# Performance work log

Hardware: AMD Instinct MI355X
Metric: run time of the kernel (lower is better)

## Reference

```python
import math
import jax, jax.numpy as jnp
import numpy as np

INPUT_SIZE = 168; PREDICT_SIZE = 168; D_MODEL = 512; D_FF = 512
WINDOW = [4, 4, 4]; INNER = 3; N_HEADS = 6; D_K = 128; N_LAYER = 6
ENC_IN = 7; D_BOTTLE = 128; T_FEAT = 4
H = N_HEADS * D_K  # 768


def _all_sizes():
    s = [INPUT_SIZE]
    for w in WINDOW:
        s.append(s[-1] // w)
    return s  # [168, 42, 10, 2]


def _enc_mask():
    # Pyraformer PAM mask: True = masked (disallowed)
    all_size = _all_sizes()
    S = sum(all_size)
    m = np.zeros((S, S), dtype=bool)
    iw = INNER // 2
    starts = np.concatenate([[0], np.cumsum(all_size)]).astype(int)
    # intra-scale neighbors
    for li, n in enumerate(all_size):
        st = starts[li]
        for i in range(st, st + n):
            l = max(i - iw, st)
            r = min(i + iw + 1, st + n)
            m[i, l:r] = True
    # inter-scale parent/child links (symmetric)
    for li in range(1, len(all_size)):
        st = starts[li]
        prev = all_size[li - 1]
        for i in range(st, st + all_size[li]):
            l = (st - prev) + (i - st) * WINDOW[li - 1]
            if i == st + all_size[li] - 1:
                r = st
            else:
                r = (st - prev) + (i - st + 1) * WINDOW[li - 1]
            m[i, l:r] = True
            m[l:r, i] = True
    return jnp.asarray(~m)


def _dec_mask():
    # get_subsequent_mask(truncate=False): query i sees all 222 encoder tokens + dec tokens 0..i
    S = sum(_all_sizes())
    q = np.arange(PREDICT_SIZE)[:, None]
    k = np.arange(S + PREDICT_SIZE)[None, :]
    return jnp.asarray(k > S + q)  # True = masked


def _pos_emb(L):
    pos = np.arange(L, dtype=np.float32)[:, None]
    div = np.exp(np.arange(0, D_MODEL, 2, dtype=np.float32) * (-math.log(10000.0) / D_MODEL))
    pe = np.zeros((L, D_MODEL), np.float32)
    pe[:, 0::2] = np.sin(pos * div)
    pe[:, 1::2] = np.cos(pos * div)
    return jnp.asarray(pe)


def _ln(x, g, b, eps):
    m = jnp.mean(x, -1, keepdims=True)
    v = jnp.mean((x - m) ** 2, -1, keepdims=True)
    return (x - m) * jax.lax.rsqrt(v + eps) * g + b


def _embed(x, t, conv_w, tw, tb):
    # TokenEmbedding: Conv1d(k=3, circular pad, no bias) + positional + TimeFeature linear
    xt = jnp.transpose(x, (0, 2, 1))  # [B,C,L]
    xt = jnp.pad(xt, ((0, 0), (0, 0), (1, 1)), mode='wrap')
    tok = jax.lax.conv_general_dilated(xt, conv_w, (1,), 'VALID',
                                       dimension_numbers=('NCH', 'OIH', 'NCH'))
    tok = jnp.transpose(tok, (0, 2, 1))  # [B,L,D]
    return tok + _pos_emb(x.shape[1])[None] + t @ tw + tb


def _mha(q_in, kv, wq, bq, wk, bk, wv, bv, wo, bo, g, b, mask):
    B, Lq, _ = q_in.shape
    Lk = kv.shape[1]
    q = (q_in @ wq + bq).reshape(B, Lq, N_HEADS, D_K)
    k = (kv @ wk + bk).reshape(B, Lk, N_HEADS, D_K)
    v = (kv @ wv + bv).reshape(B, Lk, N_HEADS, D_K)
    attn = jnp.einsum('bqhd,bkhd->bhqk', q, k) / math.sqrt(D_K)
    attn = jnp.where(mask[None, None], -1e9, attn)
    attn = jax.nn.softmax(attn, axis=-1)
    out = jnp.einsum('bhqk,bkhd->bqhd', attn, v).reshape(B, Lq, H)
    return _ln(out @ wo + bo + q_in, g, b, 1e-6)


def _ffn(x, w1, b1, w2, b2, g, b):
    h = jax.nn.gelu(x @ w1 + b1, approximate=False)
    return _ln(h @ w2 + b2 + x, g, b, 1e-6)


def _bottleneck(x, dw, db, cw, cb, bng, bnb, bnm, bnv, uw, ub, lg, lb):
    # Bottleneck_Construct: down-proj, stack of strided convs (one per window), up-proj, concat, LN
    tmp = jnp.transpose(x @ dw + db, (0, 2, 1))  # [B,128,L]
    outs = []
    for i in range(len(WINDOW)):
        tmp = jax.lax.conv_general_dilated(tmp, cw[i], (WINDOW[i],), 'VALID',
                                           dimension_numbers=('NCH', 'OIH', 'NCH'))
        tmp = tmp + cb[i][None, :, None]
        # BatchNorm1d in eval mode (running stats)
        tmp = (tmp - bnm[i][None, :, None]) * jax.lax.rsqrt(bnv[i][None, :, None] + 1e-5)
        tmp = tmp * bng[i][None, :, None] + bnb[i][None, :, None]
        tmp = jax.nn.elu(tmp)
        outs.append(tmp)
    cat = jnp.transpose(jnp.concatenate(outs, axis=2), (0, 2, 1))  # [B,54,128]
    up = cat @ uw + ub
    return _ln(jnp.concatenate([x, up], axis=1), lg, lb, 1e-5)  # [B,222,512]


def _forward(p):
    mask_e = _enc_mask()
    enc = _embed(p['x_enc'], p['t_enc'], p['enc_tok_w'], p['enc_time_w'], p['enc_time_b'])
    enc = _bottleneck(enc, p['bc_down_w'], p['bc_down_b'], p['bc_conv_w'], p['bc_conv_b'],
                      p['bc_bn_g'], p['bc_bn_b'], p['bc_bn_m'], p['bc_bn_v'],
                      p['bc_up_w'], p['bc_up_b'], p['bc_ln_g'], p['bc_ln_b'])
    for i in range(N_LAYER):
        enc = _mha(enc, enc, p['enc_wq'][i], p['enc_bq'][i], p['enc_wk'][i], p['enc_bk'][i],
                   p['enc_wv'][i], p['enc_bv'][i], p['enc_wo'][i], p['enc_bo'][i],
                   p['enc_ln1_g'][i], p['enc_ln1_b'][i], mask_e)
        enc = _ffn(enc, p['enc_w1'][i], p['enc_b1'][i], p['enc_w2'][i], p['enc_b2'][i],
                   p['enc_ln2_g'][i], p['enc_ln2_b'][i])
    dec = _embed(p['x_dec'], p['t_dec'], p['dec_tok_w'], p['dec_time_w'], p['dec_time_b'])
    mask_d = _dec_mask()
    for i in range(2):
        kv = jnp.concatenate([enc, dec], axis=1)  # [B,390,D]
        dec = _mha(dec, kv, p['dec_wq'][i], p['dec_bq'][i], p['dec_wk'][i], p['dec_bk'][i],
                   p['dec_wv'][i], p['dec_bv'][i], p['dec_wo'][i], p['dec_bo'][i],
                   p['dec_ln1_g'][i], p['dec_ln1_b'][i], mask_d)
        dec = _ffn(dec, p['dec_w1'][i], p['dec_b1'][i], p['dec_w2'][i], p['dec_b2'][i],
                   p['dec_ln2_g'][i], p['dec_ln2_b'][i])
    if p['pretrain']:
        dec = jnp.concatenate([p_enc_trunc(dec, p), dec], axis=1)
    return dec @ p['pred_w']


def setup_inputs() -> dict:
    key = jax.random.key(0)
    cnt = [0]
    def nrm(shape, s=0.02):
        cnt[0] += 1
        return jax.random.normal(jax.random.fold_in(key, cnt[0]), shape, jnp.float32) * s
    B = 64
    d = {
        'x_enc': nrm((B, INPUT_SIZE, ENC_IN), 1.0),
        't_enc': nrm((B, INPUT_SIZE, T_FEAT), 1.0),
        'x_dec': nrm((B, PREDICT_SIZE, ENC_IN), 1.0),
        't_dec': nrm((B, PREDICT_SIZE, T_FEAT), 1.0),
        'enc_tok_w': nrm((D_MODEL, ENC_IN, 3)),
        'enc_time_w': nrm((T_FEAT, D_MODEL)), 'enc_time_b': jnp.zeros((D_MODEL,), jnp.float32),
        'dec_tok_w': nrm((D_MODEL, ENC_IN, 3)),
        'dec_time_w': nrm((T_FEAT, D_MODEL)), 'dec_time_b': jnp.zeros((D_MODEL,), jnp.float32),
        'bc_down_w': nrm((D_MODEL, D_BOTTLE)), 'bc_down_b': jnp.zeros((D_BOTTLE,), jnp.float32),
        'bc_conv_w': nrm((3, D_BOTTLE, D_BOTTLE, 4)), 'bc_conv_b': jnp.zeros((3, D_BOTTLE), jnp.float32),
        'bc_bn_g': jnp.ones((3, D_BOTTLE), jnp.float32), 'bc_bn_b': jnp.zeros((3, D_BOTTLE), jnp.float32),
        'bc_bn_m': jnp.zeros((3, D_BOTTLE), jnp.float32), 'bc_bn_v': jnp.ones((3, D_BOTTLE), jnp.float32),
        'bc_up_w': nrm((D_BOTTLE, D_MODEL)), 'bc_up_b': jnp.zeros((D_MODEL,), jnp.float32),
        'bc_ln_g': jnp.ones((D_MODEL,), jnp.float32), 'bc_ln_b': jnp.zeros((D_MODEL,), jnp.float32),
    }
    for prefix, n in (('enc_', N_LAYER), ('dec_', 2)):
        d[prefix + 'wq'] = nrm((n, D_MODEL, H)); d[prefix + 'bq'] = jnp.zeros((n, H), jnp.float32)
        d[prefix + 'wk'] = nrm((n, D_MODEL, H)); d[prefix + 'bk'] = jnp.zeros((n, H), jnp.float32)
        d[prefix + 'wv'] = nrm((n, D_MODEL, H)); d[prefix + 'bv'] = jnp.zeros((n, H), jnp.float32)
        d[prefix + 'wo'] = nrm((n, H, D_MODEL)); d[prefix + 'bo'] = jnp.zeros((n, D_MODEL), jnp.float32)
        d[prefix + 'ln1_g'] = jnp.ones((n, D_MODEL), jnp.float32); d[prefix + 'ln1_b'] = jnp.zeros((n, D_MODEL), jnp.float32)
        d[prefix + 'w1'] = nrm((n, D_MODEL, D_FF)); d[prefix + 'b1'] = jnp.zeros((n, D_FF), jnp.float32)
        d[prefix + 'w2'] = nrm((n, D_FF, D_MODEL)); d[prefix + 'b2'] = jnp.zeros((n, D_MODEL), jnp.float32)
        d[prefix + 'ln2_g'] = jnp.ones((n, D_MODEL), jnp.float32); d[prefix + 'ln2_b'] = jnp.zeros((n, D_MODEL), jnp.float32)
    d['pred_w'] = nrm((D_MODEL, ENC_IN))
    d['pretrain'] = 0
    return d


def reference(x_enc, t_enc, x_dec, t_dec, enc_tok_w, enc_time_w, enc_time_b, dec_tok_w, dec_time_w, dec_time_b, bc_down_w, bc_down_b, bc_conv_w, bc_conv_b, bc_bn_g, bc_bn_b, bc_bn_m, bc_bn_v, bc_up_w, bc_up_b, bc_ln_g, bc_ln_b, enc_wq, enc_bq, enc_wk, enc_bk, enc_wv, enc_bv, enc_wo, enc_bo, enc_ln1_g, enc_ln1_b, enc_w1, enc_b1, enc_w2, enc_b2, enc_ln2_g, enc_ln2_b, dec_wq, dec_bq, dec_wk, dec_bk, dec_wv, dec_bv, dec_wo, dec_bo, dec_ln1_g, dec_ln1_b, dec_w1, dec_b1, dec_w2, dec_b2, dec_ln2_g, dec_ln2_b, pred_w, pretrain):
    p = dict(locals())
    return _forward(p)
```

## Files before the change

kernel.cpp:

```cpp
#include <hip/hip_runtime.h>
#include <cstdint>
#include <cstddef>

#define BSZ   64
#define L_IN  168
#define S1    222
#define SKV   390
#define DM    512
#define HD    768
#define NHD   6
#define DK    128

typedef unsigned short u16;
typedef unsigned int u32;
typedef __attribute__((ext_vector_type(8))) short bf16x8;
typedef __attribute__((ext_vector_type(4))) float f32x4v;

__device__ inline float b2f(u16 u){
  union { u32 i; float f; } v; v.i = ((u32)u) << 16; return v.f;
}
__device__ inline u16 f2b(float f){
  union { float f; u32 i; } v; v.f = f;
  u32 x = v.i;
  return (u16)((x + 0x7fffu + ((x >> 16) & 1u)) >> 16);
}
__device__ inline u32 pk2(float a, float b){
  return ((u32)f2b(b) << 16) | (u32)f2b(a);
}
__device__ inline float ldv(const void* p, long long i, bool f32){
  return f32 ? ((const float*)p)[i] : b2f(((const u16*)p)[i]);
}
__device__ inline float4 ldv4(const void* p, long long i, bool f32){
  if (f32) return *(const float4*)((const float*)p + i);
  ushort4 w = *(const ushort4*)((const u16*)p + i);
  return make_float4(b2f(w.x), b2f(w.y), b2f(w.z), b2f(w.w));
}
__device__ inline bool is_f32(const u16* det){ return det[0] != 0x3F80; }
__device__ inline void unpack8(uint4 w, float* f){
  union { u32 i; float fl; } a;
  a.i = w.x << 16;          f[0] = a.fl;
  a.i = w.x & 0xffff0000u;  f[1] = a.fl;
  a.i = w.y << 16;          f[2] = a.fl;
  a.i = w.y & 0xffff0000u;  f[3] = a.fl;
  a.i = w.z << 16;          f[4] = a.fl;
  a.i = w.z & 0xffff0000u;  f[5] = a.fl;
  a.i = w.w << 16;          f[6] = a.fl;
  a.i = w.w & 0xffff0000u;  f[7] = a.fl;
}

__device__ inline void gload_lds16(const void* g, void* l){
  __builtin_amdgcn_global_load_lds((const __attribute__((address_space(1))) void*)g,
                                   (__attribute__((address_space(3))) void*)l, 16, 0, 0);
}

constexpr size_t OFF_ENCX = 0;
constexpr size_t OFF_DECX = OFF_ENCX + (size_t)BSZ*S1*DM;
constexpr size_t OFF_QB   = OFF_DECX + (size_t)BSZ*L_IN*DM;
constexpr size_t OFF_KB   = OFF_QB   + (size_t)BSZ*S1*HD/2;
constexpr size_t OFF_VB   = OFF_KB   + (size_t)BSZ*SKV*HD/2;
constexpr size_t OFF_NBR  = OFF_VB   + (size_t)BSZ*SKV*HD/2;
constexpr size_t OFF_ENCB = OFF_NBR  + 4096;
constexpr size_t OFF_DECB = OFF_ENCB + (size_t)BSZ*S1*DM/2;
constexpr size_t OFF_WT   = OFF_DECB + (size_t)BSZ*L_IN*DM/2;
constexpr size_t WT_SLOT  = 2097152;
constexpr size_t WS_NEED  = (OFF_WT) * 4;
constexpr size_t WS_NEED2 = (OFF_WT + 8*WT_SLOT/2) * 4;

__device__ inline int scale_of(int i, int& ii){
  if (i < 168){ ii = i;       return 0; }
  if (i < 210){ ii = i - 168; return 1; }
  if (i < 220){ ii = i - 210; return 2; }
  ii = i - 220; return 3;
}
__device__ inline bool pam_ok(int i, int j){
  int ii, jj;
  int li = scale_of(i, ii);
  int lj = scale_of(j, jj);
  const int n[4] = {168, 42, 10, 2};
  if (li == lj){ int d = ii - jj; return (d <= 1 && d >= -1); }
  if (li == lj + 1){ int lo = ii*4, hi = (ii == n[li]-1) ? n[lj] : ii*4+4; return (jj >= lo && jj < hi); }
  if (lj == li + 1){ int lo = jj*4, hi = (jj == n[lj]-1) ? n[li] : jj*4+4; return (ii >= lo && ii < hi); }
  return false;
}
__global__ __launch_bounds__(256)
void build_nbr_kernel(int* __restrict__ nbr){
  int wid = (blockIdx.x * 256 + threadIdx.x) >> 6;
  int lane = threadIdx.x & 63;
  if (wid >= S1) return;
  int q = wid;
  int cnt = 0;
  int list[12];
  #pragma unroll
  for (int r = 0; r < 4; ++r){
    int j = r*64 + lane;
    bool ok = (j < S1) && pam_ok(q, j);
    unsigned long long m = __ballot(ok);
    while (m && cnt < 12){
      int bit = __builtin_ctzll(m);
      m &= m - 1;
      list[cnt++] = r*64 + bit;
    }
  }
  if (lane == 0){
    #pragma unroll
    for (int t = 0; t < 12; ++t) nbr[q*12 + t] = (t < cnt) ? list[t] : -1;
  }
}

__global__ __launch_bounds__(256)
void embed_fast(const void* __restrict__ x, const void* __restrict__ t,
                const void* __restrict__ cw, const void* __restrict__ tw,
                const void* __restrict__ tb, const u16* __restrict__ det,
                float* __restrict__ out, u16* __restrict__ out2)
{
  bool f32 = is_f32(det);
  int d0 = threadIdx.x;
  int d1 = threadIdx.x + 256;

  float w0[21], w1[21];
  #pragma unroll
  for (int i = 0; i < 21; ++i){
    w0[i] = ldv(cw, (long long)d0*21 + i, f32);
    w1[i] = ldv(cw, (long long)d1*21 + i, f32);
  }
  float tw0[4], tw1[4];
  #pragma unroll
  for (int f = 0; f < 4; ++f){
    tw0[f] = ldv(tw, (long long)f*DM + d0, f32);
    tw1[f] = ldv(tw, (long long)f*DM + d1, f32);
  }
  float tb0 = ldv(tb, d0, f32);
  float tb1 = ldv(tb, d1, f32);
  float dv0 = __expf(-(float)(d0 & ~1) * (9.210340371976184f/512.f));
  float dv1 = __expf(-(float)(d1 & ~1) * (9.210340371976184f/512.f));
  bool odd0 = (d0 & 1), odd1 = (d1 & 1);

  const int nRows = BSZ * L_IN;
  for (int row = blockIdx.x; row < nRows; row += gridDim.x){
    int b = row / L_IN, l = row - b*L_IN;
    float acc0 = 0.f, acc1 = 0.f;
    #pragma unroll
    for (int tt = 0; tt < 3; ++tt){
      int ls = l + tt - 1;
      ls = (ls < 0) ? ls + L_IN : (ls >= L_IN ? ls - L_IN : ls);
      long long xo = ((long long)(b*L_IN + ls))*7;
      #pragma unroll
      for (int c = 0; c < 7; ++c){
        float xv = ldv(x, xo + c, f32);
        acc0 += xv * w0[c*3 + tt];
        acc1 += xv * w1[c*3 + tt];
      }
    }
    float ang0 = (float)l * dv0;
    float ang1 = (float)l * dv1;
    acc0 += odd0 ? __cosf(ang0) : __sinf(ang0);
    acc1 += odd1 ? __cosf(ang1) : __sinf(ang1);
    long long to = ((long long)row)*4;
    #pragma unroll
    for (int f = 0; f < 4; ++f){
      float tv = ldv(t, to + f, f32);
      acc0 += tv * tw0[f];
      acc1 += tv * tw1[f];
    }
    acc0 += tb0;
    acc1 += tb1;
    size_t o = (size_t)row*DM;
    out[o + d0] = acc0;
    out[o + d1] = acc1;
    if (out2){
      out2[o + d0] = f2b(acc0);
      out2[o + d1] = f2b(acc1);
    }
  }
}

__device__ inline void trans32(const void* W, long long wOff, int K, int N, int k0, int n0,
                               u16* __restrict__ Wt, bool f32, float* tb, int tid)
{
  int c = tid & 31, r0 = tid >> 5;
  #pragma unroll
  for (int rr = 0; rr < 32; rr += 8)
    tb[(r0+rr)*33 + c] = ldv(W, wOff + (long long)(k0+r0+rr)*N + n0 + c, f32);
  __syncthreads();
  #pragma unroll
  for (int rr = 0; rr < 32; rr += 8)
    Wt[(size_t)(n0+r0+rr)*K + k0 + c] = f2b(tb[c*33 + r0+rr]);
}

__device__ inline void wt_layer_body(int t, const void* wq, const void* wk, const void* wv,
                                     const void* wo, const void* w1, const void* w2,
                                     long long wO, long long oO, long long fO,
                                     u16* Wt3, u16* WtO, u16* Wt1, u16* Wt2,
                                     bool f32, float* tb, int tid)
{
  if (t < 384)       trans32(wq, wO, 512, 768, (t/24)*32, (t%24)*32, Wt3,               f32, tb, tid);
  else if (t < 768)  { int u = t-384;  trans32(wk, wO, 512, 768, (u/24)*32, (u%24)*32, Wt3 + (size_t)768*512,  f32, tb, tid); }
  else if (t < 1152) { int u = t-768;  trans32(wv, wO, 512, 768, (u/24)*32, (u%24)*32, Wt3 + (size_t)1536*512, f32, tb, tid); }
  else if (t < 1536) { int u = t-1152; trans32(wo, oO, 768, 512, (u/16)*32, (u%16)*32, WtO, f32, tb, tid); }
  else if (t < 1792) { int u = t-1536; trans32(w1, fO, 512, 512, (u/16)*32, (u%16)*32, Wt1, f32, tb, tid); }
  else               { int u = t-1792; trans32(w2, fO, 512, 512, (u/16)*32, (u%16)*32, Wt2, f32, tb, tid); }
}

__global__ __launch_bounds__(256)
void wt_batch(const void* wq, const void* wk, const void* wv,
              const void* wo, const void* w1, const void* w2,
              long long wO, long long oO, long long fO,
              u16* __restrict__ Wt3, u16* __restrict__ WtO,
              u16* __restrict__ Wt1, u16* __restrict__ Wt2,
              const u16* __restrict__ det)
{
  __shared__ float tb[32*33];
  bool f32 = is_f32(det);
  wt_layer_body(blockIdx.x, wq, wk, wv, wo, w1, w2, wO, oO, fO, Wt3, WtO, Wt1, Wt2,
                f32, tb, threadIdx.x);
}

__global__ __launch_bounds__(256)
void wt_all(const void* ewq, const void* ewk, const void* ewv, const void* ewo,
            const void* ew1, const void* ew2,
            const void* dwq, const void* dwk, const void* dwv, const void* dwo,
            const void* dw1, const void* dw2,
            u16* __restrict__ WtAll, const u16* __restrict__ det)
{
  __shared__ float tb[32*33];
  bool f32 = is_f32(det);
  int s = blockIdx.x >> 11;
  int t = blockIdx.x & 2047;
  bool enc = s < 6;
  int li = enc ? s : s - 6;
  long long wO = (long long)li*512*768, oO = (long long)li*768*512, fO = (long long)li*512*512;
  u16* base = WtAll + (size_t)s*WT_SLOT;
  wt_layer_body(t,
                enc ? ewq : dwq, enc ? ewk : dwk, enc ? ewv : dwv,
                enc ? ewo : dwo, enc ? ew1 : dw1, enc ? ew2 : dw2,
                wO, oO, fO,
                base, base + (size_t)2304*512,
                base + (size_t)2304*512 + (size_t)512*768,
                base + (size_t)2304*512 + (size_t)512*768 + (size_t)512*512,
                f32, tb, threadIdx.x);
}

template<int CN>
__device__ inline bool swzT(int t, int RP, int CP, int rpx, int& row0, int& col0){
  int xcd = t & 7, j = t >> 3;
  int rp = xcd + 8*(j % rpx);
  int cp = j / rpx;
  if (rp >= RP || cp >= CP) return false;
  row0 = rp*128; col0 = cp*CN;
  return true;
}

template<int EPI, int ABF, int CBF, int CN>
__global__ __launch_bounds__(256)
void gemm_mfma(const void* __restrict__ Av, const u16* __restrict__ Wt,
               const void* __restrict__ bias, long long bOff, const float* __restrict__ R,
               void* __restrict__ Cv, const u16* __restrict__ det,
               int K, int N, int La, int Lc, int off, int RP, int CP, int rpx)
{
  constexpr int NF = CN/32;
  __shared__ u16 As[128][64];
  __shared__ u16 Bs[CN][64];
  bool f32 = is_f32(det);
  int tid = threadIdx.x;
  int row0, col0;
  if (!swzT<CN>(blockIdx.x, RP, CP, rpx, row0, col0)) return;
  int wave = tid >> 6, lane = tid & 63;
  int wm = (wave >> 1)*64, wn = (wave & 1)*(CN/2);
  int lm = lane & 15, quad = lane >> 4;
  int sr = tid >> 1;
  int sh = (tid & 1) * 32;
  int swzS = (sr & 7) * 8;
  int r8 = lane >> 3;
  int scw = ((lane & 7)*8) ^ (r8*8);
  f32x4v acc[4][NF];
  #pragma unroll
  for (int i = 0; i < 4; ++i)
    #pragma unroll
    for (int j = 0; j < NF; ++j) acc[i][j] = (f32x4v){0.f,0.f,0.f,0.f};

  for (int k0 = 0; k0 < K; k0 += 64){
    if (ABF){
      const u16* base = (const u16*)Av + (size_t)row0*K + k0 + scw;
      #pragma unroll
      for (int j = 0; j < 4; ++j){
        int r = wave*32 + j*8;
        gload_lds16(base + (size_t)(r + r8)*K, &As[r][0]);
      }
    } else {
      const float* src = (const float*)Av + (size_t)(row0+sr)*K + k0 + sh;
      #pragma unroll
      for (int j = 0; j < 4; ++j){
        float4 f0 = *(const float4*)(src + 8*j);
        float4 f1 = *(const float4*)(src + 8*j + 4);
        uint4 o;
        o.x = pk2(f0.x, f0.y); o.y = pk2(f0.z, f0.w);
        o.z = pk2(f1.x, f1.y); o.w = pk2(f1.z, f1.w);
        *(uint4*)&As[sr][(sh + 8*j)^swzS] = o;
      }
    }
    {
      const u16* base = Wt + (size_t)col0*K + k0 + scw;
      #pragma unroll
      for (int j = 0; j < CN/32; ++j){
        int r = wave*(CN/4) + j*8;
        gload_lds16(base + (size_t)(r + r8)*K, &Bs[r][0]);
      }
    }
    __syncthreads();
    bf16x8 af[4][2], bfr[NF][2];
    #pragma unroll
    for (int mi = 0; mi < 4; ++mi){
      int m = wm + mi*16 + lm;
      int sz = (m & 7)*8;
      af[mi][0] = *(const bf16x8*)&As[m][(quad*8) ^ sz];
      af[mi][1] = *(const bf16x8*)&As[m][(32 + quad*8) ^ sz];
    }
    #pragma unroll
    for (int ni = 0; ni < NF; ++ni){
      int n = wn + ni*16 + lm;
      int sz = (n & 7)*8;
      bfr[ni][0] = *(const bf16x8*)&Bs[n][(quad*8) ^ sz];
      bfr[ni][1] = *(const bf16x8*)&Bs[n][(32 + quad*8) ^ sz];
    }
    #pragma unroll
    for (int mi = 0; mi < 4; ++mi)
      #pragma unroll
      for (int ni = 0; ni < NF; ++ni){
        acc[mi][ni] = __builtin_amdgcn_mfma_f32_16x16x32_bf16(af[mi][0], bfr[ni][0], acc[mi][ni], 0, 0, 0);
        acc[mi][ni] = __builtin_amdgcn_mfma_f32_16x16x32_bf16(af[mi][1], bfr[ni][1], acc[mi][ni], 0, 0, 0);
      }
    __syncthreads();
  }
  #pragma unroll
  for (int mi = 0; mi < 4; ++mi){
    #pragma unroll
    for (int r = 0; r < 4; ++r){
      int row = row0 + wm + mi*16 + quad*4 + r;
      int bb = row / La, l = row - bb*La;
      size_t crow = ((size_t)bb*Lc + off + l)*(size_t)N;
      #pragma unroll
      for (int ni = 0; ni < NF; ++ni){
        int col = col0 + wn + ni*16 + lm;
        float vv = acc[mi][ni][r] + ldv(bias, bOff + col, f32);
        if (EPI == 1) vv = 0.5f*vv*(1.f + erff(vv*0.70710678118654752f));
        if (EPI == 2) vv += R[crow + col];
        if (CBF) ((u16*)Cv)[crow + col] = f2b(vv);
        else     ((float*)Cv)[crow + col] = vv;
      }
    }
  }
}

template<int ABF, int CN>
__global__ __launch_bounds__(256)
void gemm_qkv(const void* __restrict__ Av, const u16* __restrict__ Wt,
              const void* __restrict__ b0, const void* __restrict__ b1, const void* __restrict__ b2,
              long long bOff, u16* __restrict__ o0, u16* __restrict__ o1, u16* __restrict__ o2,
              const u16* __restrict__ det, int La, int Lc, int off, int RP, int CP, int rpx)
{
  constexpr int NF = CN/32;
  __shared__ u16 As[128][64];
  __shared__ u16 Bs[CN][64];
  bool f32 = is_f32(det);
  const int K = 512;
  int tid = threadIdx.x;
  int row0, col0;
  if (!swzT<CN>(blockIdx.x, RP, CP, rpx, row0, col0)) return;
  int wave = tid >> 6, lane = tid & 63;
  int wm = (wave >> 1)*64, wn = (wave & 1)*(CN/2);
  int lm = lane & 15, quad = lane >> 4;
  int sr = tid >> 1;
  int sh = (tid & 1) * 32;
  int swzS = (sr & 7) * 8;
  int r8 = lane >> 3;
  int scw = ((lane & 7)*8) ^ (r8*8);
  f32x4v acc[4][NF];
  #pragma unroll
  for (int i = 0; i < 4; ++i)
    #pragma unroll
    for (int j = 0; j < NF; ++j) acc[i][j] = (f32x4v){0.f,0.f,0.f,0.f};

  for (int k0 = 0; k0 < K; k0 += 64){
    if (ABF){
      const u16* base = (const u16*)Av + (size_t)row0*K + k0 + scw;
      #pragma unroll
      for (int j = 0; j < 4; ++j){
        int r = wave*32 + j*8;
        gload_lds16(base + (size_t)(r + r8)*K, &As[r][0]);
      }
    } else {
      const float* src = (const float*)Av + (size_t)(row0+sr)*K + k0 + sh;
      #pragma unroll
      for (int j = 0; j < 4; ++j){
        float4 f0 = *(const float4*)(src + 8*j);
        float4 f1 = *(const float4*)(src + 8*j + 4);
        uint4 o;
        o.x = pk2(f0.x, f0.y); o.y = pk2(f0.z, f0.w);
        o.z = pk2(f1.x, f1.y); o.w = pk2(f1.z, f1.w);
        *(uint4*)&As[sr][(sh + 8*j)^swzS] = o;
      }
    }
    {
      const u16* base = Wt + (size_t)col0*K + k0 + scw;
      #pragma unroll
      for (int j = 0; j < CN/32; ++j){
        int r = wave*(CN/4) + j*8;
        gload_lds16(base + (size_t)(r + r8)*K, &Bs[r][0]);
      }
    }
    __syncthreads();
    bf16x8 af[4][2], bfr[NF][2];
    #pragma unroll
    for (int mi = 0; mi < 4; ++mi){
      int m = wm + mi*16 + lm;
      int sz = (m & 7)*8;
      af[mi][0] = *(const bf16x8*)&As[m][(quad*8) ^ sz];
      af[mi][1] = *(const bf16x8*)&As[m][(32 + quad*8) ^ sz];
    }
    #pragma unroll
    for (int ni = 0; ni < NF; ++ni){
      int n = wn + ni*16 + lm;
      int sz = (n & 7)*8;
      bfr[ni][0] = *(const bf16x8*)&Bs[n][(quad*8) ^ sz];
      bfr[ni][1] = *(const bf16x8*)&Bs[n][(32 + quad*8) ^ sz];
    }
    #pragma unroll
    for (int mi = 0; mi < 4; ++mi)
      #pragma unroll
      for (int ni = 0; ni < NF; ++ni){
        acc[mi][ni] = __builtin_amdgcn_mfma_f32_16x16x32_bf16(af[mi][0], bfr[ni][0], acc[mi][ni], 0, 0, 0);
        acc[mi][ni] = __builtin_amdgcn_mfma_f32_16x16x32_bf16(af[mi][1], bfr[ni][1], acc[mi][ni], 0, 0, 0);
      }
    __syncthreads();
  }
  #pragma unroll
  for (int mi = 0; mi < 4; ++mi){
    #pragma unroll
    for (int r = 0; r < 4; ++r){
      int row = row0 + wm + mi*16 + quad*4 + r;
      int bb = row / La, l = row - bb*La;
      size_t crow = ((size_t)bb*Lc + off + l)*(size_t)HD;
      #pragma unroll
      for (int ni = 0; ni < NF; ++ni){
        int col = col0 + wn + ni*16 + lm;
        int sel = (col >= 1536) ? 2 : (col >= 768 ? 1 : 0);
        int colr = col - sel*768;
        const void* bp = (sel == 0) ? b0 : (sel == 1) ? b1 : b2;
        u16* dst = (sel == 0) ? o0 : (sel == 1) ? o1 : o2;
        float vv = acc[mi][ni][r] + ldv(bp, bOff + colr, f32);
        dst[crow + colr] = f2b(vv);
      }
    }
  }
}

#define BM 64
#define BN 64
#define BK 16
__global__ __launch_bounds__(256)
void gemm_k(const float* __restrict__ A, const void* __restrict__ W, long long wOff,
            const void* __restrict__ bias, long long bOff,
            float* __restrict__ C, const u16* __restrict__ det, int K, int N)
{
  __shared__ float As2[BK][BM+4];
  __shared__ float Bs2[BK][BN+4];
  bool f32 = is_f32(det);
  int tid = threadIdx.x;
  int row0 = blockIdx.y * BM, col0 = blockIdx.x * BN;
  int ty = tid >> 4, tx = tid & 15;
  int lr = tid >> 2, lc4 = (tid & 3) << 2;
  int wr = tid >> 4, wc4 = (tid & 15) << 2;
  float acc[4][4] = {};
  for (int k0 = 0; k0 < K; k0 += BK){
    float4 av = *(const float4*)(A + (size_t)(row0 + lr)*K + k0 + lc4);
    As2[lc4+0][lr] = av.x; As2[lc4+1][lr] = av.y;
    As2[lc4+2][lr] = av.z; As2[lc4+3][lr] = av.w;
    float4 wv = ldv4(W, wOff + (long long)(k0 + wr)*N + col0 + wc4, f32);
    *(float4*)&Bs2[wr][wc4] = wv;
    __syncthreads();
    #pragma unroll
    for (int kk = 0; kk < BK; ++kk){
      float4 a  = *(const float4*)&As2[kk][ty << 2];
      float4 bb = *(const float4*)&Bs2[kk][tx << 2];
      acc[0][0] += a.x*bb.x; acc[0][1] += a.x*bb.y; acc[0][2] += a.x*bb.z; acc[0][3] += a.x*bb.w;
      acc[1][0] += a.y*bb.x; acc[1][1] += a.y*bb.y; acc[1][2] += a.y*bb.z; acc[1][3] += a.y*bb.w;
      acc[2][0] += a.z*bb.x; acc[2][1] += a.z*bb.y; acc[2][2] += a.z*bb.z; acc[2][3] += a.z*bb.w;
      acc[3][0] += a.w*bb.x; acc[3][1] += a.w*bb.y; acc[3][2] += a.w*bb.z; acc[3][3] += a.w*bb.w;
    }
    __syncthreads();
  }
  #pragma unroll
  for (int i = 0; i < 4; ++i){
    int r = row0 + (ty << 2) + i;
    size_t crow = (size_t)r*(size_t)N;
    #pragma unroll
    for (int j = 0; j < 4; ++j){
      int c = col0 + (tx << 2) + j;
      C[crow + c] = acc[i][j] + ldv(bias, bOff + c, f32);
    }
  }
}

__global__ void wc_kernel(const void* __restrict__ w, float* __restrict__ Wc,
                          const u16* __restrict__ det)
{
  bool f32 = is_f32(det);
  int idx = blockIdx.x * 256 + threadIdx.x;
  if (idx >= 3*512*128) return;
  int co = idx & 127;
  int kk = (idx >> 7) & 511;
  int lay = idx >> 16;
  int tt = kk >> 7, ci = kk & 127;
  Wc[idx] = ldv(w, (long long)lay*65536 + co*512 + ci*4 + tt, f32);
}

__global__ __launch_bounds__(256)
void conv_gemm(const float* __restrict__ in, int inStride, int inOff,
               float* __restrict__ out, int outStride, int outOff, int Lout,
               const float* __restrict__ Wc,
               const void* __restrict__ cb, const void* __restrict__ bg,
               const void* __restrict__ bb, const void* __restrict__ bm,
               const void* __restrict__ bv, const u16* __restrict__ det, int lay)
{
  __shared__ float As2[BK][BM+4];
  __shared__ float Bs2[BK][BN+4];
  bool f32 = is_f32(det);
  int tid = threadIdx.x;
  int row0 = blockIdx.y * BM, col0 = blockIdx.x * BN;
  int ty = tid >> 4, tx = tid & 15;
  int lr = tid >> 2, lc4 = (tid & 3) << 2;
  int wr = tid >> 4, wc4 = (tid & 15) << 2;
  int rs = row0 + lr;
  int bs = rs / Lout, js = rs - bs*Lout;
  const float* arow = in + ((size_t)(bs*inStride + inOff + js*4))*128;
  float acc[4][4] = {};
  for (int k0 = 0; k0 < 512; k0 += BK){
    float4 av = *(const float4*)(arow + k0 + lc4);
    As2[lc4+0][lr] = av.x; As2[lc4+1][lr] = av.y;
    As2[lc4+2][lr] = av.z; As2[lc4+3][lr] = av.w;
    float4 wv = *(const float4*)(Wc + (size_t)(k0 + wr)*128 + col0 + wc4);
    *(float4*)&Bs2[wr][wc4] = wv;
    __syncthreads();
    #pragma unroll
    for (int kk = 0; kk < BK; ++kk){
      float4 a  = *(const float4*)&As2[kk][ty << 2];
      float4 bb2 = *(const float4*)&Bs2[kk][tx << 2];
      acc[0][0] += a.x*bb2.x; acc[0][1] += a.x*bb2.y; acc[0][2] += a.x*bb2.z; acc[0][3] += a.x*bb2.w;
      acc[1][0] += a.y*bb2.x; acc[1][1] += a.y*bb2.y; acc[1][2] += a.y*bb2.z; acc[1][3] += a.y*bb2.w;
      acc[2][0] += a.z*bb2.x; acc[2][1] += a.z*bb2.y; acc[2][2] += a.z*bb2.z; acc[2][3] += a.z*bb2.w;
      acc[3][0] += a.w*bb2.x; acc[3][1] += a.w*bb2.y; acc[3][2] += a.w*bb2.z; acc[3][3] += a.w*bb2.w;
    }
    __syncthreads();
  }
  #pragma unroll
  for (int i = 0; i < 4; ++i){
    int r = row0 + (ty << 2) + i;
    int b = r / Lout, j = r - b*Lout;
    float* orow = out + ((size_t)(b*outStride + outOff + j))*128;
    #pragma unroll
    for (int jj = 0; jj < 4; ++jj){
      int co = col0 + (tx << 2) + jj;
      long long po = (long long)lay*128 + co;
      float a = acc[i][jj] + ldv(cb, po, f32);
      a = (a - ldv(bm, po, f32)) * rsqrtf(ldv(bv, po, f32) + 1e-5f) * ldv(bg, po, f32) + ldv(bb, po, f32);
      a = a > 0.f ? a : (__expf(a) - 1.f);
      orow[co] = a;
    }
  }
}

__global__ __launch_bounds__(256)
void ln_kernel(const float* __restrict__ X, const void* __restrict__ g, long long gOff,
               const void* __restrict__ bt, long long bOff, float eps,
               float* __restrict__ Out, u16* __restrict__ OutB, const u16* __restrict__ det)
{
  bool f32 = is_f32(det);
  int row = blockIdx.x*4 + (threadIdx.x >> 6);
  int lane = threadIdx.x & 63;
  const float* xr = X + (size_t)row*DM;
  float v[8]; float s = 0.f;
  #pragma unroll
  for (int i = 0; i < 8; ++i){ v[i] = xr[lane + i*64]; s += v[i]; }
  #pragma unroll
  for (int o = 32; o > 0; o >>= 1) s += __shfl_xor(s, o);
  float mean = s * (1.f/512.f);
  float q = 0.f;
  #pragma unroll
  for (int i = 0; i < 8; ++i){ float d = v[i]-mean; q += d*d; }
  #pragma unroll
  for (int o = 32; o > 0; o >>= 1) q += __shfl_xor(q, o);
  float inv = rsqrtf(q*(1.f/512.f) + eps);
  float* orow = Out + (size_t)row*DM;
  #pragma unroll
  for (int i = 0; i < 8; ++i){
    int c = lane + i*64;
    float val = (v[i]-mean)*inv*ldv(g, gOff + c, f32) + ldv(bt, bOff + c, f32);
    orow[c] = val;
    if (OutB) OutB[(size_t)row*DM + c] = f2b(val);
  }
}

__global__ __launch_bounds__(256)
void concat_ln_kernel(const float* __restrict__ emb, const float* __restrict__ up,
                      const void* __restrict__ g, const void* __restrict__ bt,
                      float* __restrict__ Out, u16* __restrict__ OutB, const u16* __restrict__ det)
{
  bool f32 = is_f32(det);
  int row = blockIdx.x*4 + (threadIdx.x >> 6);
  int lane = threadIdx.x & 63;
  int b = row / S1, l = row - b*S1;
  const float* xr = (l < L_IN) ? emb + ((size_t)(b*L_IN + l))*DM
                               : up  + ((size_t)(b*54 + (l - L_IN)))*DM;
  float v[8]; float s = 0.f;
  #pragma unroll
  for (int i = 0; i < 8; ++i){ v[i] = xr[lane + i*64]; s += v[i]; }
  #pragma unroll
  for (int o = 32; o > 0; o >>= 1) s += __shfl_xor(s, o);
  float mean = s * (1.f/512.f);
  float q = 0.f;
  #pragma unroll
  for (int i = 0; i < 8; ++i){ float d = v[i]-mean; q += d*d; }
  #pragma unroll
  for (int o = 32; o > 0; o >>= 1) q += __shfl_xor(q, o);
  float inv = rsqrtf(q*(1.f/512.f) + 1e-5f);
  float* orow = Out + (size_t)row*DM;
  #pragma unroll
  for (int i = 0; i < 8; ++i){
    int c = lane + i*64;
    float val = (v[i]-mean)*inv*ldv(g, c, f32) + ldv(bt, c, f32);
    orow[c] = val;
    if (OutB) OutB[(size_t)row*DM + c] = f2b(val);
  }
}

__global__ __launch_bounds__(256)
void attn_enc_sparse(u16* __restrict__ q, const u16* __restrict__ k,
                     const u16* __restrict__ v, const int* __restrict__ nbr)
{
  int u = blockIdx.x * 16 + (threadIdx.x >> 4);
  int lane16 = threadIdx.x & 15;
  int h = u % NHD;
  int bq = u / NHD;
  int b = bq / S1, qr = bq - b*S1;
  const float scale = 0.088388347648318447f;
  size_t rowoff = (size_t)bq*HD + h*DK + lane16*8;
  uint4 qw = *(const uint4*)(q + rowoff);
  float qd[8]; unpack8(qw, qd);
  const int* nb = nbr + qr*12;
  size_t base = (size_t)b*S1*HD + h*DK + lane16*8;
  float pj[12];
  #pragma unroll
  for (int j = 0; j < 12; ++j){
    int kg = nb[j];
    int kgc = kg < 0 ? 0 : kg;
    uint4 kw = *(const uint4*)(k + (size_t)kgc*HD + base);
    float kd[8]; unpack8(kw, kd);
    float p = qd[0]*kd[0] + qd[1]*kd[1] + qd[2]*kd[2] + qd[3]*kd[3]
            + qd[4]*kd[4] + qd[5]*kd[5] + qd[6]*kd[6] + qd[7]*kd[7];
    p += __shfl_xor(p, 1); p += __shfl_xor(p, 2);
    p += __shfl_xor(p, 4); p += __shfl_xor(p, 8);
    pj[j] = (kg >= 0) ? p*scale : -1e30f;
  }
  float m = -1e30f;
  #pragma unroll
  for (int j = 0; j < 12; ++j) m = fmaxf(m, pj[j]);
  float s = 0.f;
  #pragma unroll
  for (int j = 0; j < 12; ++j){ pj[j] = __expf(pj[j] - m); s += pj[j]; }
  float inv = 1.f / s;
  float o[8];
  #pragma unroll
  for (int i = 0; i < 8; ++i) o[i] = 0.f;
  #pragma unroll
  for (int j = 0; j < 12; ++j){
    int kg = nb[j];
    int kgc = kg < 0 ? 0 : kg;
    uint4 vw = *(const uint4*)(v + (size_t)kgc*HD + base);
    float vd[8]; unpack8(vw, vd);
    #pragma unroll
    for (int i = 0; i < 8; ++i) o[i] += pj[j]*vd[i];
  }
  uint4 ow;
  ow.x = pk2(o[0]*inv, o[1]*inv);
  ow.y = pk2(o[2]*inv, o[3]*inv);
  ow.z = pk2(o[4]*inv, o[5]*inv);
  ow.w = pk2(o[6]*inv, o[7]*inv);
  *(uint4*)(q + rowoff) = ow;
}

#define FQT 64
__global__ __launch_bounds__(256)
void attn_dec_mfma(u16* __restrict__ q, const u16* __restrict__ k,
                   const u16* __restrict__ v)
{
  __shared__ __align__(16) u16 Ks[32][136];
  __shared__ __align__(16) u32 Vt[16][132];
  __shared__ __align__(16) u32 Pls[4][16][16];
  int id = blockIdx.x;
  int qt = id / 384;
  int rem = id - qt*384;
  int h = rem >> 6;
  int b = rem & 63;
  int qt0 = qt * FQT;
  int tid = threadIdx.x;
  int wave = tid >> 6, lane = tid & 63;
  int lm = lane & 15, quad = lane >> 4;
  const float scale = 0.088388347648318447f;
  const size_t qb0 = (size_t)b*L_IN*HD + (size_t)h*DK;
  const size_t kb0 = (size_t)b*SKV*HD + (size_t)h*DK;

  bf16x8 qf[4];
  {
    int qg = qt0 + wave*16 + lm;
    if (qg < L_IN){
      #pragma unroll
      for (int ks = 0; ks < 4; ++ks)
        qf[ks] = *(const bf16x8*)(q + qb0 + (size_t)qg*HD + ks*32 + quad*8);
    } else {
      #pragma unroll
      for (int ks = 0; ks < 4; ++ks) qf[ks] = (bf16x8){0,0,0,0,0,0,0,0};
    }
  }

  float mold[4], lsum[4];
  #pragma unroll
  for (int r = 0; r < 4; ++r){ mold[r] = -1e30f; lsum[r] = 0.f; }
  f32x4v oacc[8];
  #pragma unroll
  for (int f = 0; f < 8; ++f) oacc[f] = (f32x4v){0.f,0.f,0.f,0.f};

  int kEnd = S1 + qt0 + FQT; if (kEnd > SKV) kEnd = SKV;
  int nt = (kEnd + 31) >> 5;

  ushort4 kr[4];
  ushort4 vr[2][2];
  {
// ... 322 lines not shown
```

Measured before the change: 2.410 ms.

## Double-buffer LDS tiles in GEMM kernels to overlap loads with MFMA

Both the generic GEMM and the fused QKV GEMM now keep two LDS buffers for the A and B tiles. The next K-slice is issued into the alternate buffer before the current slice's fragment reads and MFMAs run, with one barrier per iteration instead of two. The aim is to hide global-to-LDS latency behind matrix compute. In exchange LDS use doubles, which can lower occupancy, and correctness relies on the async gload_lds writes being visible by the barrier at the end of each iteration.

```diff
diff --git a/kernel.cpp b/kernel.cpp
--- a/kernel.cpp
+++ b/kernel.cpp
@@ -258,8 +258,8 @@
                int K, int N, int La, int Lc, int off, int RP, int CP, int rpx)
 {
   constexpr int NF = CN/32;
-  __shared__ u16 As[128][64];
-  __shared__ u16 Bs[CN][64];
+  __shared__ u16 As[2][128][64];
+  __shared__ u16 Bs[2][CN][64];
   bool f32 = is_f32(det);
   int tid = threadIdx.x;
   int row0, col0;
@@ -272,19 +272,14 @@
   int swzS = (sr & 7) * 8;
   int r8 = lane >> 3;
   int scw = ((lane & 7)*8) ^ (r8*8);
-  f32x4v acc[4][NF];
-  #pragma unroll
-  for (int i = 0; i < 4; ++i)
-    #pragma unroll
-    for (int j = 0; j < NF; ++j) acc[i][j] = (f32x4v){0.f,0.f,0.f,0.f};
-
-  for (int k0 = 0; k0 < K; k0 += 64){
+
+  auto stageAB = [&](int buf, int k0){
     if (ABF){
       const u16* base = (const u16*)Av + (size_t)row0*K + k0 + scw;
       #pragma unroll
       for (int j = 0; j < 4; ++j){
         int r = wave*32 + j*8;
-        gload_lds16(base + (size_t)(r + r8)*K, &As[r][0]);
+        gload_lds16(base + (size_t)(r + r8)*K, &As[buf][r][0]);
       }
     } else {
       const float* src = (const float*)Av + (size_t)(row0+sr)*K + k0 + sh;
@@ -295,32 +290,42 @@
         uint4 o;
         o.x = pk2(f0.x, f0.y); o.y = pk2(f0.z, f0.w);
         o.z = pk2(f1.x, f1.y); o.w = pk2(f1.z, f1.w);
-        *(uint4*)&As[sr][(sh + 8*j)^swzS] = o;
-      }
-    }
-    {
-      const u16* base = Wt + (size_t)col0*K + k0 + scw;
-      #pragma unroll
-      for (int j = 0; j < CN/32; ++j){
-        int r = wave*(CN/4) + j*8;
-        gload_lds16(base + (size_t)(r + r8)*K, &Bs[r][0]);
-      }
-    }
-    __syncthreads();
+        *(uint4*)&As[buf][sr][(sh + 8*j)^swzS] = o;
+      }
+    }
+    const u16* wbase = Wt + (size_t)col0*K + k0 + scw;
+    #pragma unroll
+    for (int j = 0; j < CN/32; ++j){
+      int r = wave*(CN/4) + j*8;
+      gload_lds16(wbase + (size_t)(r + r8)*K, &Bs[buf][r][0]);
+    }
+  };
+
+  f32x4v acc[4][NF];
+  #pragma unroll
+  for (int i = 0; i < 4; ++i)
+    #pragma unroll
+    for (int j = 0; j < NF; ++j) acc[i][j] = (f32x4v){0.f,0.f,0.f,0.f};
+
+  stageAB(0, 0);
+  __syncthreads();
+  int cur = 0;
+  for (int k0 = 0; k0 < K; k0 += 64){
+    if (k0 + 64 < K) stageAB(cur ^ 1, k0 + 64);
     bf16x8 af[4][2], bfr[NF][2];
     #pragma unroll
     for (int mi = 0; mi < 4; ++mi){
       int m = wm + mi*16 + lm;
       int sz = (m & 7)*8;
-      af[mi][0] = *(const bf16x8*)&As[m][(quad*8) ^ sz];
-      af[mi][1] = *(const bf16x8*)&As[m][(32 + quad*8) ^ sz];
+      af[mi][0] = *(const bf16x8*)&As[cur][m][(quad*8) ^ sz];
+      af[mi][1] = *(const bf16x8*)&As[cur][m][(32 + quad*8) ^ sz];
     }
     #pragma unroll
     for (int ni = 0; ni < NF; ++ni){
       int n = wn + ni*16 + lm;
       int sz = (n & 7)*8;
-      bfr[ni][0] = *(const bf16x8*)&Bs[n][(quad*8) ^ sz];
-      bfr[ni][1] = *(const bf16x8*)&Bs[n][(32 + quad*8) ^ sz];
+      bfr[ni][0] = *(const bf16x8*)&Bs[cur][n][(quad*8) ^ sz];
+      bfr[ni][1] = *(const bf16x8*)&Bs[cur][n][(32 + quad*8) ^ sz];
     }
     #pragma unroll
     for (int mi = 0; mi < 4; ++mi)
@@ -330,6 +335,7 @@
         acc[mi][ni] = __builtin_amdgcn_mfma_f32_16x16x32_bf16(af[mi][1], bfr[ni][1], acc[mi][ni], 0, 0, 0);
       }
     __syncthreads();
+    cur ^= 1;
   }
   #pragma unroll
   for (int mi = 0; mi < 4; ++mi){
@@ -359,8 +365,8 @@
               const u16* __restrict__ det, int La, int Lc, int off, int RP, int CP, int rpx)
 {
   constexpr int NF = CN/32;
-  __shared__ u16 As[128][64];
-  __shared__ u16 Bs[CN][64];
+  __shared__ u16 As[2][128][64];
+  __shared__ u16 Bs[2][CN][64];
   bool f32 = is_f32(det);
   const int K = 512;
   int tid = threadIdx.x;
@@ -374,19 +380,14 @@
   int swzS = (sr & 7) * 8;
   int r8 = lane >> 3;
   int scw = ((lane & 7)*8) ^ (r8*8);
-  f32x4v acc[4][NF];
-  #pragma unroll
-  for (int i = 0; i < 4; ++i)
-    #pragma unroll
-    for (int j = 0; j < NF; ++j) acc[i][j] = (f32x4v){0.f,0.f,0.f,0.f};
-
-  for (int k0 = 0; k0 < K; k0 += 64){
+
+  auto stageAB = [&](int buf, int k0){
     if (ABF){
       const u16* base = (const u16*)Av + (size_t)row0*K + k0 + scw;
       #pragma unroll
       for (int j = 0; j < 4; ++j){
         int r = wave*32 + j*8;
-        gload_lds16(base + (size_t)(r + r8)*K, &As[r][0]);
+        gload_lds16(base + (size_t)(r + r8)*K, &As[buf][r][0]);
       }
     } else {
       const float* src = (const float*)Av + (size_t)(row0+sr)*K + k0 + sh;
@@ -397,32 +398,42 @@
         uint4 o;
         o.x = pk2(f0.x, f0.y); o.y = pk2(f0.z, f0.w);
         o.z = pk2(f1.x, f1.y); o.w = pk2(f1.z, f1.w);
-        *(uint4*)&As[sr][(sh + 8*j)^swzS] = o;
-      }
-    }
-    {
-      const u16* base = Wt + (size_t)col0*K + k0 + scw;
-      #pragma unroll
-      for (int j = 0; j < CN/32; ++j){
-        int r = wave*(CN/4) + j*8;
-        gload_lds16(base + (size_t)(r + r8)*K, &Bs[r][0]);
-      }
-    }
-    __syncthreads();
+        *(uint4*)&As[buf][sr][(sh + 8*j)^swzS] = o;
+      }
+    }
+    const u16* wbase = Wt + (size_t)col0*K + k0 + scw;
+    #pragma unroll
+    for (int j = 0; j < CN/32; ++j){
+      int r = wave*(CN/4) + j*8;
+      gload_lds16(wbase + (size_t)(r + r8)*K, &Bs[buf][r][0]);
+    }
+  };
+
+  f32x4v acc[4][NF];
+  #pragma unroll
+  for (int i = 0; i < 4; ++i)
+    #pragma unroll
+    for (int j = 0; j < NF; ++j) acc[i][j] = (f32x4v){0.f,0.f,0.f,0.f};
+
+  stageAB(0, 0);
+  __syncthreads();
+  int cur = 0;
+  for (int k0 = 0; k0 < K; k0 += 64){
+    if (k0 + 64 < K) stageAB(cur ^ 1, k0 + 64);
     bf16x8 af[4][2], bfr[NF][2];
     #pragma unroll
     for (int mi = 0; mi < 4; ++mi){
       int m = wm + mi*16 + lm;
       int sz = (m & 7)*8;
-      af[mi][0] = *(const bf16x8*)&As[m][(quad*8) ^ sz];
-      af[mi][1] = *(const bf16x8*)&As[m][(32 + quad*8) ^ sz];
+      af[mi][0] = *(const bf16x8*)&As[cur][m][(quad*8) ^ sz];
+      af[mi][1] = *(const bf16x8*)&As[cur][m][(32 + quad*8) ^ sz];
     }
     #pragma unroll
     for (int ni = 0; ni < NF; ++ni){
       int n = wn + ni*16 + lm;
       int sz = (n & 7)*8;
-      bfr[ni][0] = *(const bf16x8*)&Bs[n][(quad*8) ^ sz];
-      bfr[ni][1] = *(const bf16x8*)&Bs[n][(32 + quad*8) ^ sz];
+      bfr[ni][0] = *(const bf16x8*)&Bs[cur][n][(quad*8) ^ sz];
+      bfr[ni][1] = *(const bf16x8*)&Bs[cur][n][(32 + quad*8) ^ sz];
     }
     #pragma unroll
     for (int mi = 0; mi < 4; ++mi)
@@ -432,6 +443,7 @@
         acc[mi][ni] = __builtin_amdgcn_mfma_f32_16x16x32_bf16(af[mi][1], bfr[ni][1], acc[mi][ni], 0, 0, 0);
       }
     __syncthreads();
+    cur ^= 1;
   }
   #pragma unroll
   for (int mi = 0; mi < 4; ++mi){
```

After: 2.798 ms. 16.1% more time.
